# Kernel optimization log

Measured on AMD Instinct MI355X. Metric: run time of the kernel, lower is better.

The kernel has to match this reference:

```python
import jax, jax.numpy as jnp
import numpy as np

B, T, IN_DIM = 128, 4096, 13
UNITS, MOTOR = 64, 6
LAYERS = [35, 23, 6]   # AutoNCP(64, 6): inter / command / motor neurons
_SPLITS = [35, 58]     # cumulative layer boundaries inside the 64-unit state


def setup_inputs() -> dict:
    keys = iter(jax.random.split(jax.random.key(0), 64))
    def rn(shape, s=0.1):
        return jax.random.normal(next(keys), shape, dtype=jnp.float32) * s
    inp = {"x": jax.random.normal(next(keys), (B, T, IN_DIM), dtype=jnp.float32)}
    # mixed-memory LSTM cell (ncps: input_map has bias, recurrent_map does not)
    inp["lstm_wi"] = rn((4 * UNITS, IN_DIM))
    inp["lstm_wh"] = rn((4 * UNITS, UNITS))
    inp["lstm_b"] = rn((4 * UNITS,))
    # wired CfC layers: ff1/ff2/time_a/time_b acting on concat([input, h])
    in_dims = [IN_DIM] + LAYERS[:-1]
    for i, (d, h) in enumerate(zip(in_dims, LAYERS)):
        for nm in ("w1", "w2", "wa", "wb"):
            inp[f"cfc{i}_{nm}"] = rn((h, d + h))
        for nm in ("b1", "b2", "ba", "bb"):
            inp[f"cfc{i}_{nm}"] = rn((h,))
    inp["gyro_w1"] = rn((32, MOTOR)); inp["gyro_b1"] = rn((32,))
    inp["gyro_w2"] = rn((3, 32));     inp["gyro_b2"] = rn((3,))
    inp["acc_w1"] = rn((32, MOTOR));  inp["acc_b1"] = rn((32,))
    inp["acc_w2"] = rn((3, 32));      inp["acc_b2"] = rn((3,))
    inp["unc_w1"] = rn((16, MOTOR));  inp["unc_b1"] = rn((16,))
    inp["unc_w2"] = rn((6, 16));      inp["unc_b2"] = rn((6,))
    return inp


def _cfc_step(inp, h, p):
    """ncps CfCCell, mode='default', no backbone, ts = 1.0."""
    W1, b1, W2, b2, Wa, ba, Wb, bb = p
    z = jnp.concatenate([inp, h], axis=-1)            # (B, in+hid)
    ff1 = jnp.tanh(z @ W1.T + b1)
    ff2 = jnp.tanh(z @ W2.T + b2)
    t = jax.nn.sigmoid((z @ Wa.T + ba) + (z @ Wb.T + bb))  # t_a*ts + t_b, ts==1
    return ff1 * (1.0 - t) + t * ff2


def reference(x, lstm_wi, lstm_wh, lstm_b,
              cfc0_w1, cfc0_b1, cfc0_w2, cfc0_b2, cfc0_wa, cfc0_ba, cfc0_wb, cfc0_bb,
              cfc1_w1, cfc1_b1, cfc1_w2, cfc1_b2, cfc1_wa, cfc1_ba, cfc1_wb, cfc1_bb,
              cfc2_w1, cfc2_b1, cfc2_w2, cfc2_b2, cfc2_wa, cfc2_ba, cfc2_wb, cfc2_bb,
              gyro_w1, gyro_b1, gyro_w2, gyro_b2,
              acc_w1, acc_b1, acc_w2, acc_b2,
              unc_w1, unc_b1, unc_w2, unc_b2):
    layer_params = (
        (cfc0_w1, cfc0_b1, cfc0_w2, cfc0_b2, cfc0_wa, cfc0_ba, cfc0_wb, cfc0_bb),
        (cfc1_w1, cfc1_b1, cfc1_w2, cfc1_b2, cfc1_wa, cfc1_ba, cfc1_wb, cfc1_bb),
        (cfc2_w1, cfc2_b1, cfc2_w2, cfc2_b2, cfc2_wa, cfc2_ba, cfc2_wb, cfc2_bb),
    )

    def step(carry, xt):  # xt: (B, 13)
        h, c = carry
        # mixed-memory LSTM over the full 64-unit state (forget gate +1.0)
        zg = xt @ lstm_wi.T + lstm_b + h @ lstm_wh.T
        ia, ig, fg, og = jnp.split(zg, 4, axis=-1)
        c_new = c * jax.nn.sigmoid(fg + 1.0) + jnp.tanh(ia) * jax.nn.sigmoid(ig)
        h_lstm = jnp.tanh(c_new) * jax.nn.sigmoid(og)
        # wired CfC: inter -> command -> motor, each fed previous layer's output
        hs = jnp.split(h_lstm, _SPLITS, axis=-1)
        inp = xt
        new_hs = []
        for hi, p in zip(hs, layer_params):
            inp = _cfc_step(inp, hi, p)
            new_hs.append(inp)
        return (jnp.concatenate(new_hs, axis=-1), c_new), inp  # motor out (B,6)

    Bsz = x.shape[0]
    h0 = jnp.zeros((Bsz, UNITS), x.dtype)
    c0 = jnp.zeros((Bsz, UNITS), x.dtype)
    _, outs = jax.lax.scan(step, (h0, c0), jnp.swapaxes(x, 0, 1))
    cfc_out = jnp.swapaxes(outs, 0, 1)  # (B, T, 6)

    gyro = jnp.tanh(cfc_out @ gyro_w1.T + gyro_b1) @ gyro_w2.T + gyro_b2
    acc = jnp.tanh(cfc_out @ acc_w1.T + acc_b1) @ acc_w2.T + acc_b2
    pred = jnp.concatenate([gyro, acc], axis=-1)                      # (B, T, 6)
    unc = jax.nn.softplus(
        jax.nn.relu(cfc_out @ unc_w1.T + unc_b1) @ unc_w2.T + unc_b2)  # (B, T, 6)
    return pred, unc
```

## Files before the change

kernel.cpp:

```cpp
#include <hip/hip_runtime.h>
#include <math.h>

#define BATCH 128
#define TSTEPS 4096
#define INDIM 13


__device__ __forceinline__ float fsig(float x) {
    return __builtin_amdgcn_rcpf(1.f + __expf(-x));
}
__device__ __forceinline__ float ftanh(float x) {
    float s = fsig(x + x);
    return s + s - 1.f;
}
__device__ __forceinline__ float fsoftplus(float x) {
    return (x > 15.f) ? x : __logf(1.f + __expf(x));
}

#define BFLY(a) { a += __shfl_xor(a, 1, 64); a += __shfl_xor(a, 2, 64); }

#define FMA4(acc, W, q, zv) { acc += zv.x * W##_##q##_0; acc += zv.y * W##_##q##_1; \
                              acc += zv.z * W##_##q##_2; acc += zv.w * W##_##q##_3; }

__global__ __attribute__((amdgpu_flat_work_group_size(256, 256),
                          amdgpu_waves_per_eu(1, 1)))
void rnn_kernel(const float* __restrict__ x,
                const float* __restrict__ lstm_wi, const float* __restrict__ lstm_wh,
                const float* __restrict__ lstm_b,
                const float* __restrict__ c0w1, const float* __restrict__ c0w2,
                const float* __restrict__ c0wa, const float* __restrict__ c0wb,
                const float* __restrict__ c0b1, const float* __restrict__ c0b2,
                const float* __restrict__ c0ba, const float* __restrict__ c0bb,
                const float* __restrict__ c1w1, const float* __restrict__ c1w2,
                const float* __restrict__ c1wa, const float* __restrict__ c1wb,
                const float* __restrict__ c1b1, const float* __restrict__ c1b2,
                const float* __restrict__ c1ba, const float* __restrict__ c1bb,
                const float* __restrict__ c2w1, const float* __restrict__ c2w2,
                const float* __restrict__ c2wa, const float* __restrict__ c2wb,
                const float* __restrict__ c2b1, const float* __restrict__ c2b2,
                const float* __restrict__ c2ba, const float* __restrict__ c2bb,
                float* __restrict__ out)
{
    const int bb = blockIdx.x;
    const int t  = threadIdx.x;
    const int g  = t & 3;
    const int u  = t >> 2;

    __shared__ __align__(16) float smem[224];
    float* zL = smem;
    float* z0 = smem + 80;
    float* z1 = smem + 128;
    float* z2 = smem + 192;

    const long xbase = (long)bb * TSTEPS * INDIM;
    const long obase = (long)bb * TSTEPS * 6;

    auto lwf = [&](int A, int c) -> float {
        int r = A * 64 + u;
        return (c < 13) ? lstm_wi[r * 13 + c]
             : (c < 77) ? lstm_wh[r * 64 + (c - 13)] : 0.f;
    };
#define DEF_WL(A,q) \
    float wl##A##_##q##_0 = lwf(A, 20*g + 4*q + 0); \
    float wl##A##_##q##_1 = lwf(A, 20*g + 4*q + 1); \
    float wl##A##_##q##_2 = lwf(A, 20*g + 4*q + 2); \
    float wl##A##_##q##_3 = lwf(A, 20*g + 4*q + 3);
    DEF_WL(0,0) DEF_WL(0,1) DEF_WL(0,2) DEF_WL(0,3) DEF_WL(0,4)
    DEF_WL(1,0) DEF_WL(1,1) DEF_WL(1,2) DEF_WL(1,3) DEF_WL(1,4)
    DEF_WL(2,0) DEF_WL(2,1) DEF_WL(2,2) DEF_WL(2,3) DEF_WL(2,4)
    DEF_WL(3,0) DEF_WL(3,1) DEF_WL(3,2) DEF_WL(3,3) DEF_WL(3,4)
#undef DEF_WL
    const float bL0 = lstm_b[u];
    const float bL1 = lstm_b[64 + u];
    const float bL2 = lstm_b[128 + u];
    const float bL3 = lstm_b[192 + u];

    const int grp = (t < 140) ? 0 : (t < 232) ? 1 : 2;
    const int row = (grp == 0) ? u : (grp == 1) ? (u - 35) : (u - 58);
    const int rl  = (grp == 0) ? 48 : (grp == 1) ? 58 : 29;
    const int cb  = (grp == 0) ? 12 * g : (grp == 1) ? 16 * g : 8 * g;
    const float *W0p, *W1p, *W2p, *W3p;
    float bC0, bC1, bC2, bC3;
    if (grp == 0) {
        W0p = c0w1 + row * 48; W1p = c0w2 + row * 48;
        W2p = c0wa + row * 48; W3p = c0wb + row * 48;
        bC0 = c0b1[row]; bC1 = c0b2[row]; bC2 = c0ba[row]; bC3 = c0bb[row];
    } else if (grp == 1) {
        W0p = c1w1 + row * 58; W1p = c1w2 + row * 58;
        W2p = c1wa + row * 58; W3p = c1wb + row * 58;
        bC0 = c1b1[row]; bC1 = c1b2[row]; bC2 = c1ba[row]; bC3 = c1bb[row];
    } else {
        W0p = c2w1 + row * 29; W1p = c2w2 + row * 29;
        W2p = c2wa + row * 29; W3p = c2wb + row * 29;
        bC0 = c2b1[row]; bC1 = c2b2[row]; bC2 = c2ba[row]; bC3 = c2bb[row];
    }
    auto cwf = [&](const float* W, int c) -> float {
        int cc = cb + c;
        return (cc < rl) ? W[cc] : 0.f;
    };
#define DEF_WC(A,q) \
    float wc##A##_##q##_0 = cwf(W##A##p, 4*q + 0); \
    float wc##A##_##q##_1 = cwf(W##A##p, 4*q + 1); \
    float wc##A##_##q##_2 = cwf(W##A##p, 4*q + 2); \
    float wc##A##_##q##_3 = cwf(W##A##p, 4*q + 3);
    DEF_WC(0,0) DEF_WC(0,1) DEF_WC(0,2) DEF_WC(0,3)
    DEF_WC(1,0) DEF_WC(1,1) DEF_WC(1,2) DEF_WC(1,3)
    DEF_WC(2,0) DEF_WC(2,1) DEF_WC(2,2) DEF_WC(2,3)
    DEF_WC(3,0) DEF_WC(3,1) DEF_WC(3,2) DEF_WC(3,3)
#undef DEF_WC

    const bool pfl = (t >= 96 && t < 109);
    float creg = 0.f;

    if (t >= 13 && t < 224) smem[t] = 0.f;
    if (t < 13)             zL[t] = x[xbase + t];
    __syncthreads();

    #pragma unroll 1
    for (int ts = 0; ts < TSTEPS; ++ts) {
        float xn = 0.f;
        if (pfl && (ts + 1) < TSTEPS)
            xn = x[xbase + (long)(ts + 1) * 13 + (t - 96)];
        if (g == 1 && u < 13) z0[u] = zL[u];
        {
            const float4* zc = (const float4*)(zL + 20 * g);
            float4 q0 = zc[0], q1 = zc[1], q2 = zc[2], q3 = zc[3], q4 = zc[4];
            float a0 = 0.f, a1 = 0.f, a2 = 0.f, a3 = 0.f;
            FMA4(a0, wl0, 0, q0) FMA4(a0, wl0, 1, q1) FMA4(a0, wl0, 2, q2)
            FMA4(a0, wl0, 3, q3) FMA4(a0, wl0, 4, q4)
            FMA4(a1, wl1, 0, q0) FMA4(a1, wl1, 1, q1) FMA4(a1, wl1, 2, q2)
            FMA4(a1, wl1, 3, q3) FMA4(a1, wl1, 4, q4)
            FMA4(a2, wl2, 0, q0) FMA4(a2, wl2, 1, q1) FMA4(a2, wl2, 2, q2)
            FMA4(a2, wl2, 3, q3) FMA4(a2, wl2, 4, q4)
            FMA4(a3, wl3, 0, q0) FMA4(a3, wl3, 1, q1) FMA4(a3, wl3, 2, q2)
            FMA4(a3, wl3, 3, q3) FMA4(a3, wl3, 4, q4)
            BFLY(a0) BFLY(a1) BFLY(a2) BFLY(a3)
            a0 += bL0; a1 += bL1; a2 += bL2; a3 += bL3;
            float cn = creg * fsig(a2 + 1.f) + ftanh(a0) * fsig(a1);
            creg = cn;
            float hl = ftanh(cn) * fsig(a3);
            if (g == 0) {
                if (u < 35)      z0[13 + u] = hl;
                else if (u < 58) z1[u]      = hl;
                else             z2[u - 35] = hl;
            }
        }
        __syncthreads();

        if (grp == 0) {
            const float4* zc = (const float4*)(z0 + 12 * g);
            float4 p0 = zc[0], p1 = zc[1], p2 = zc[2];
            float a0 = 0.f, a1 = 0.f, a2 = 0.f, a3 = 0.f;
            FMA4(a0, wc0, 0, p0) FMA4(a0, wc0, 1, p1) FMA4(a0, wc0, 2, p2)
            FMA4(a1, wc1, 0, p0) FMA4(a1, wc1, 1, p1) FMA4(a1, wc1, 2, p2)
            FMA4(a2, wc2, 0, p0) FMA4(a2, wc2, 1, p1) FMA4(a2, wc2, 2, p2)
            FMA4(a3, wc3, 0, p0) FMA4(a3, wc3, 1, p1) FMA4(a3, wc3, 2, p2)
            BFLY(a0) BFLY(a1) BFLY(a2) BFLY(a3)
            a0 += bC0; a1 += bC1; a2 += bC2; a3 += bC3;
            float tg = fsig(a2 + a3);
            float f1 = ftanh(a0), f2 = ftanh(a1);
            float o = f1 + tg * (f2 - f1);
            if (g == 0) { z1[row] = o; zL[13 + row] = o; }
        }
        __syncthreads();

        if (grp == 1) {
            const float4* zc = (const float4*)(z1 + 16 * g);
            float4 p0 = zc[0], p1 = zc[1], p2 = zc[2], p3 = zc[3];
            float a0 = 0.f, a1 = 0.f, a2 = 0.f, a3 = 0.f;
            FMA4(a0, wc0, 0, p0) FMA4(a0, wc0, 1, p1) FMA4(a0, wc0, 2, p2) FMA4(a0, wc0, 3, p3)
            FMA4(a1, wc1, 0, p0) FMA4(a1, wc1, 1, p1) FMA4(a1, wc1, 2, p2) FMA4(a1, wc1, 3, p3)
            FMA4(a2, wc2, 0, p0) FMA4(a2, wc2, 1, p1) FMA4(a2, wc2, 2, p2) FMA4(a2, wc2, 3, p3)
            FMA4(a3, wc3, 0, p0) FMA4(a3, wc3, 1, p1) FMA4(a3, wc3, 2, p2) FMA4(a3, wc3, 3, p3)
            BFLY(a0) BFLY(a1) BFLY(a2) BFLY(a3)
            a0 += bC0; a1 += bC1; a2 += bC2; a3 += bC3;
            float tg = fsig(a2 + a3);
            float f1 = ftanh(a0), f2 = ftanh(a1);
            float o = f1 + tg * (f2 - f1);
            if (g == 0) { z2[row] = o; zL[48 + row] = o; }
        }
        __syncthreads();

        if (grp == 2) {
            const float4* zc = (const float4*)(z2 + 8 * g);
            float4 p0 = zc[0], p1 = zc[1];
            float a0 = 0.f, a1 = 0.f, a2 = 0.f, a3 = 0.f;
            FMA4(a0, wc0, 0, p0) FMA4(a0, wc0, 1, p1)
            FMA4(a1, wc1, 0, p0) FMA4(a1, wc1, 1, p1)
            FMA4(a2, wc2, 0, p0) FMA4(a2, wc2, 1, p1)
            FMA4(a3, wc3, 0, p0) FMA4(a3, wc3, 1, p1)
            BFLY(a0) BFLY(a1) BFLY(a2) BFLY(a3)
            a0 += bC0; a1 += bC1; a2 += bC2; a3 += bC3;
            float tg = fsig(a2 + a3);
            float f1 = ftanh(a0), f2 = ftanh(a1);
            float o = f1 + tg * (f2 - f1);
            if (g == 0) {
                out[obase + (long)ts * 6 + row] = o;
                zL[71 + row] = o;
            }
        } else if (pfl) {
            zL[t - 96] = xn;
        }
        __syncthreads();
    }
}

#define S_GW1 0
#define S_GB1 192
#define S_GW2 224
#define S_GB2 320
#define S_AW1 323
#define S_AB1 515
#define S_AW2 547
#define S_AB2 643
#define S_UW1 646
#define S_UB1 742
#define S_UW2 758
#define S_UB2 854
#define S_TOT 860

__global__ __launch_bounds__(256)
void head_kernel(const float* __restrict__ gw1, const float* __restrict__ gb1,
                 const float* __restrict__ gw2, const float* __restrict__ gb2,
                 const float* __restrict__ aw1, const float* __restrict__ ab1,
                 const float* __restrict__ aw2, const float* __restrict__ ab2,
                 const float* __restrict__ uw1, const float* __restrict__ ub1,
                 const float* __restrict__ uw2, const float* __restrict__ ub2,
                 float* __restrict__ out)
{
    __shared__ float s[S_TOT];
    const int t = threadIdx.x;
    if (t < 192) { s[S_GW1 + t] = gw1[t]; s[S_AW1 + t] = aw1[t]; }
    if (t < 96)  { s[S_GW2 + t] = gw2[t]; s[S_AW2 + t] = aw2[t];
                   s[S_UW1 + t] = uw1[t]; s[S_UW2 + t] = uw2[t]; }
    if (t < 32)  { s[S_GB1 + t] = gb1[t]; s[S_AB1 + t] = ab1[t]; }
    if (t < 16)  { s[S_UB1 + t] = ub1[t]; }
    if (t < 3)   { s[S_GB2 + t] = gb2[t]; s[S_AB2 + t] = ab2[t]; }
    if (t < 6)   { s[S_UB2 + t] = ub2[t]; }
    __syncthreads();

    const long p = (long)blockIdx.x * 256 + t;
    const long base = p * 6;
    float m0 = out[base+0], m1 = out[base+1], m2 = out[base+2];
    float m3 = out[base+3], m4 = out[base+4], m5 = out[base+5];

    float gy0 = s[S_GB2+0], gy1 = s[S_GB2+1], gy2 = s[S_GB2+2];
    float ac0 = s[S_AB2+0], ac1 = s[S_AB2+1], ac2 = s[S_AB2+2];
    #pragma unroll
    for (int i = 0; i < 32; ++i) {
        float hg = s[S_GB1+i] + s[S_GW1+i*6+0]*m0 + s[S_GW1+i*6+1]*m1
                 + s[S_GW1+i*6+2]*m2 + s[S_GW1+i*6+3]*m3
                 + s[S_GW1+i*6+4]*m4 + s[S_GW1+i*6+5]*m5;
        hg = ftanh(hg);
        gy0 += s[S_GW2+i]*hg; gy1 += s[S_GW2+32+i]*hg; gy2 += s[S_GW2+64+i]*hg;
        float ha = s[S_AB1+i] + s[S_AW1+i*6+0]*m0 + s[S_AW1+i*6+1]*m1
                 + s[S_AW1+i*6+2]*m2 + s[S_AW1+i*6+3]*m3
                 + s[S_AW1+i*6+4]*m4 + s[S_AW1+i*6+5]*m5;
        ha = ftanh(ha);
        ac0 += s[S_AW2+i]*ha; ac1 += s[S_AW2+32+i]*ha; ac2 += s[S_AW2+64+i]*ha;
    }
    float u0 = s[S_UB2+0], u1 = s[S_UB2+1], u2 = s[S_UB2+2];
    float u3 = s[S_UB2+3], u4 = s[S_UB2+4], u5 = s[S_UB2+5];
    #pragma unroll
    for (int i = 0; i < 16; ++i) {
        float hu = s[S_UB1+i] + s[S_UW1+i*6+0]*m0 + s[S_UW1+i*6+1]*m1
                 + s[S_UW1+i*6+2]*m2 + s[S_UW1+i*6+3]*m3
                 + s[S_UW1+i*6+4]*m4 + s[S_UW1+i*6+5]*m5;
        hu = fmaxf(hu, 0.f);
        u0 += s[S_UW2+i]*hu;      u1 += s[S_UW2+16+i]*hu; u2 += s[S_UW2+32+i]*hu;
        u3 += s[S_UW2+48+i]*hu;   u4 += s[S_UW2+64+i]*hu; u5 += s[S_UW2+80+i]*hu;
    }
    out[base+0] = gy0; out[base+1] = gy1; out[base+2] = gy2;
    out[base+3] = ac0; out[base+4] = ac1; out[base+5] = ac2;
    const long uoff = (long)BATCH * TSTEPS * 6;
    out[uoff+base+0] = fsoftplus(u0); out[uoff+base+1] = fsoftplus(u1);
    out[uoff+base+2] = fsoftplus(u2); out[uoff+base+3] = fsoftplus(u3);
    out[uoff+base+4] = fsoftplus(u4); out[uoff+base+5] = fsoftplus(u5);
}

extern "C" void kernel_launch(void* const* d_in, const int* in_sizes, int n_in,
                              void* d_out, int out_size, void* d_ws, size_t ws_size,
                              hipStream_t stream) {
    const float* x       = (const float*)d_in[0];
    const float* lstm_wi = (const float*)d_in[1];
    const float* lstm_wh = (const float*)d_in[2];
    const float* lstm_b  = (const float*)d_in[3];
    const float* c0w1 = (const float*)d_in[4];
    const float* c0w2 = (const float*)d_in[5];
    const float* c0wa = (const float*)d_in[6];
    const float* c0wb = (const float*)d_in[7];
    const float* c0b1 = (const float*)d_in[8];
    const float* c0b2 = (const float*)d_in[9];
    const float* c0ba = (const float*)d_in[10];
    const float* c0bb = (const float*)d_in[11];
    const float* c1w1 = (const float*)d_in[12];
    const float* c1w2 = (const float*)d_in[13];
    const float* c1wa = (const float*)d_in[14];
    const float* c1wb = (const float*)d_in[15];
    const float* c1b1 = (const float*)d_in[16];
    const float* c1b2 = (const float*)d_in[17];
    const float* c1ba = (const float*)d_in[18];
    const float* c1bb = (const float*)d_in[19];
    const float* c2w1 = (const float*)d_in[20];
    const float* c2w2 = (const float*)d_in[21];
    const float* c2wa = (const float*)d_in[22];
    const float* c2wb = (const float*)d_in[23];
    const float* c2b1 = (const float*)d_in[24];
    const float* c2b2 = (const float*)d_in[25];
    const float* c2ba = (const float*)d_in[26];
    const float* c2bb = (const float*)d_in[27];
    const float* gw1 = (const float*)d_in[28];
    const float* gb1 = (const float*)d_in[29];
    const float* gw2 = (const float*)d_in[30];
    const float* gb2 = (const float*)d_in[31];
    const float* aw1 = (const float*)d_in[32];
    const float* ab1 = (const float*)d_in[33];
    const float* aw2 = (const float*)d_in[34];
    const float* ab2 = (const float*)d_in[35];
    const float* uw1 = (const float*)d_in[36];
    const float* ub1 = (const float*)d_in[37];
    const float* uw2 = (const float*)d_in[38];
    const float* ub2 = (const float*)d_in[39];
    float* out = (float*)d_out;

    rnn_kernel<<<BATCH, 256, 0, stream>>>(x, lstm_wi, lstm_wh, lstm_b,
        c0w1, c0w2, c0wa, c0wb, c0b1, c0b2, c0ba, c0bb,
        c1w1, c1w2, c1wa, c1wb, c1b1, c1b2, c1ba, c1bb,
        c2w1, c2w2, c2wa, c2wb, c2b1, c2b2, c2ba, c2bb, out);

    head_kernel<<<(BATCH * TSTEPS) / 256, 256, 0, stream>>>(
        gw1, gb1, gw2, gb2, aw1, ab1, aw2, ab2, uw1, ub1, uw2, ub2, out);
}
```

Before: 6.448 ms.

## Split each unit's dot products across 8 lanes with DPP/swizzle reductions

Doubles the block to 512 threads so each hidden unit's LSTM and CfC dot products are split across 8 lanes instead of 4. This shortens the serial FMA chain per lane in every recurrent step. The 3-step shuffle reduction uses DPP quad permutes plus a ds_swizzle in place of __shfl_xor. The cost is twice as many waves synchronising at each of the four barriers per timestep, and one extra reduction stage.

```diff
diff --git a/kernel.cpp b/kernel.cpp
--- a/kernel.cpp
+++ b/kernel.cpp
@@ -17,13 +17,24 @@
     return (x > 15.f) ? x : __logf(1.f + __expf(x));
 }
 
-#define BFLY(a) { a += __shfl_xor(a, 1, 64); a += __shfl_xor(a, 2, 64); }
+__device__ __forceinline__ float qxor1(float v) {
+    return __int_as_float(__builtin_amdgcn_update_dpp(
+        0, __float_as_int(v), 0xB1, 0xF, 0xF, true));
+}
+__device__ __forceinline__ float qxor2(float v) {
+    return __int_as_float(__builtin_amdgcn_update_dpp(
+        0, __float_as_int(v), 0x4E, 0xF, 0xF, true));
+}
+__device__ __forceinline__ float sxor4(float v) {
+    return __int_as_float(__builtin_amdgcn_ds_swizzle(
+        __float_as_int(v), 0x101F));
+}
+#define BFLY8(a) { a += sxor4(a); a += qxor2(a); a += qxor1(a); }
 
 #define FMA4(acc, W, q, zv) { acc += zv.x * W##_##q##_0; acc += zv.y * W##_##q##_1; \
                               acc += zv.z * W##_##q##_2; acc += zv.w * W##_##q##_3; }
 
-__global__ __attribute__((amdgpu_flat_work_group_size(256, 256),
-                          amdgpu_waves_per_eu(1, 1)))
+__global__ __launch_bounds__(512, 2)
 void rnn_kernel(const float* __restrict__ x,
                 const float* __restrict__ lstm_wi, const float* __restrict__ lstm_wh,
                 const float* __restrict__ lstm_b,
@@ -43,14 +54,14 @@
 {
     const int bb = blockIdx.x;
     const int t  = threadIdx.x;
-    const int g  = t & 3;
-    const int u  = t >> 2;
-
-    __shared__ __align__(16) float smem[224];
+    const int k  = t & 7;
+    const int u  = t >> 3;
+
+    __shared__ __align__(16) float smem[256];
     float* zL = smem;
-    float* z0 = smem + 80;
-    float* z1 = smem + 128;
-    float* z2 = smem + 192;
+    float* z0 = smem + 96;
+    float* z1 = smem + 160;
+    float* z2 = smem + 224;
 
     const long xbase = (long)bb * TSTEPS * INDIM;
     const long obase = (long)bb * TSTEPS * 6;
@@ -61,24 +72,25 @@
              : (c < 77) ? lstm_wh[r * 64 + (c - 13)] : 0.f;
     };
 #define DEF_WL(A,q) \
-    float wl##A##_##q##_0 = lwf(A, 20*g + 4*q + 0); \
-    float wl##A##_##q##_1 = lwf(A, 20*g + 4*q + 1); \
-    float wl##A##_##q##_2 = lwf(A, 20*g + 4*q + 2); \
-    float wl##A##_##q##_3 = lwf(A, 20*g + 4*q + 3);
-    DEF_WL(0,0) DEF_WL(0,1) DEF_WL(0,2) DEF_WL(0,3) DEF_WL(0,4)
-    DEF_WL(1,0) DEF_WL(1,1) DEF_WL(1,2) DEF_WL(1,3) DEF_WL(1,4)
-    DEF_WL(2,0) DEF_WL(2,1) DEF_WL(2,2) DEF_WL(2,3) DEF_WL(2,4)
-    DEF_WL(3,0) DEF_WL(3,1) DEF_WL(3,2) DEF_WL(3,3) DEF_WL(3,4)
+    float wl##A##_##q##_0 = lwf(A, 12*k + 4*q + 0); \
+    float wl##A##_##q##_1 = lwf(A, 12*k + 4*q + 1); \
+    float wl##A##_##q##_2 = lwf(A, 12*k + 4*q + 2); \
+    float wl##A##_##q##_3 = lwf(A, 12*k + 4*q + 3);
+    DEF_WL(0,0) DEF_WL(0,1) DEF_WL(0,2)
+    DEF_WL(1,0) DEF_WL(1,1) DEF_WL(1,2)
+    DEF_WL(2,0) DEF_WL(2,1) DEF_WL(2,2)
+    DEF_WL(3,0) DEF_WL(3,1) DEF_WL(3,2)
 #undef DEF_WL
     const float bL0 = lstm_b[u];
     const float bL1 = lstm_b[64 + u];
     const float bL2 = lstm_b[128 + u];
     const float bL3 = lstm_b[192 + u];
 
-    const int grp = (t < 140) ? 0 : (t < 232) ? 1 : 2;
-    const int row = (grp == 0) ? u : (grp == 1) ? (u - 35) : (u - 58);
-    const int rl  = (grp == 0) ? 48 : (grp == 1) ? 58 : 29;
-    const int cb  = (grp == 0) ? 12 * g : (grp == 1) ? 16 * g : 8 * g;
+    const int grp  = (u < 35) ? 0 : (u < 58) ? 1 : 2;
+    const int row  = (grp == 0) ? u : (grp == 1) ? (u - 35) : (u - 58);
+    const int rl   = (grp == 0) ? 48 : (grp == 1) ? 58 : 29;
+    const int clen = (grp == 2) ? 4 : 8;
+    const int cb   = (grp == 2) ? 4 * k : 8 * k;
     const float *W0p, *W1p, *W2p, *W3p;
     float bC0, bC1, bC2, bC3;
     if (grp == 0) {
@@ -96,50 +108,47 @@
     }
     auto cwf = [&](const float* W, int c) -> float {
         int cc = cb + c;
-        return (cc < rl) ? W[cc] : 0.f;
+        return (c < clen && cc < rl) ? W[cc] : 0.f;
     };
 #define DEF_WC(A,q) \
     float wc##A##_##q##_0 = cwf(W##A##p, 4*q + 0); \
     float wc##A##_##q##_1 = cwf(W##A##p, 4*q + 1); \
     float wc##A##_##q##_2 = cwf(W##A##p, 4*q + 2); \
     float wc##A##_##q##_3 = cwf(W##A##p, 4*q + 3);
-    DEF_WC(0,0) DEF_WC(0,1) DEF_WC(0,2) DEF_WC(0,3)
-    DEF_WC(1,0) DEF_WC(1,1) DEF_WC(1,2) DEF_WC(1,3)
-    DEF_WC(2,0) DEF_WC(2,1) DEF_WC(2,2) DEF_WC(2,3)
-    DEF_WC(3,0) DEF_WC(3,1) DEF_WC(3,2) DEF_WC(3,3)
+    DEF_WC(0,0) DEF_WC(0,1)
+    DEF_WC(1,0) DEF_WC(1,1)
+    DEF_WC(2,0) DEF_WC(2,1)
+    DEF_WC(3,0) DEF_WC(3,1)
 #undef DEF_WC
 
-    const bool pfl = (t >= 96 && t < 109);
+    const bool pfl = (t >= 128 && t < 141);
     float creg = 0.f;
 
-    if (t >= 13 && t < 224) smem[t] = 0.f;
-    if (t < 13)             zL[t] = x[xbase + t];
+    if (t < 256) smem[t] = 0.f;
+    __syncthreads();
+    if (t < 13) zL[t] = x[xbase + t];
     __syncthreads();
 
     #pragma unroll 1
     for (int ts = 0; ts < TSTEPS; ++ts) {
         float xn = 0.f;
         if (pfl && (ts + 1) < TSTEPS)
-            xn = x[xbase + (long)(ts + 1) * 13 + (t - 96)];
-        if (g == 1 && u < 13) z0[u] = zL[u];
+            xn = x[xbase + (long)(ts + 1) * 13 + (t - 128)];
+        if (t >= 256 && t < 269) z0[t - 256] = zL[t - 256];
         {
-            const float4* zc = (const float4*)(zL + 20 * g);
-            float4 q0 = zc[0], q1 = zc[1], q2 = zc[2], q3 = zc[3], q4 = zc[4];
+            const float4* zc = (const float4*)(zL + 12 * k);
+            float4 q0 = zc[0], q1 = zc[1], q2 = zc[2];
             float a0 = 0.f, a1 = 0.f, a2 = 0.f, a3 = 0.f;
             FMA4(a0, wl0, 0, q0) FMA4(a0, wl0, 1, q1) FMA4(a0, wl0, 2, q2)
-            FMA4(a0, wl0, 3, q3) FMA4(a0, wl0, 4, q4)
             FMA4(a1, wl1, 0, q0) FMA4(a1, wl1, 1, q1) FMA4(a1, wl1, 2, q2)
-            FMA4(a1, wl1, 3, q3) FMA4(a1, wl1, 4, q4)
             FMA4(a2, wl2, 0, q0) FMA4(a2, wl2, 1, q1) FMA4(a2, wl2, 2, q2)
-            FMA4(a2, wl2, 3, q3) FMA4(a2, wl2, 4, q4)
             FMA4(a3, wl3, 0, q0) FMA4(a3, wl3, 1, q1) FMA4(a3, wl3, 2, q2)
-            FMA4(a3, wl3, 3, q3) FMA4(a3, wl3, 4, q4)
-            BFLY(a0) BFLY(a1) BFLY(a2) BFLY(a3)
+            BFLY8(a0) BFLY8(a1) BFLY8(a2) BFLY8(a3)
             a0 += bL0; a1 += bL1; a2 += bL2; a3 += bL3;
             float cn = creg * fsig(a2 + 1.f) + ftanh(a0) * fsig(a1);
             creg = cn;
             float hl = ftanh(cn) * fsig(a3);
-            if (g == 0) {
+            if (k == 0) {
                 if (u < 35)      z0[13 + u] = hl;
                 else if (u < 58) z1[u]      = hl;
                 else             z2[u - 35] = hl;
@@ -148,58 +157,58 @@
         __syncthreads();
 
         if (grp == 0) {
-            const float4* zc = (const float4*)(z0 + 12 * g);
-            float4 p0 = zc[0], p1 = zc[1], p2 = zc[2];
-            float a0 = 0.f, a1 = 0.f, a2 = 0.f, a3 = 0.f;
-            FMA4(a0, wc0, 0, p0) FMA4(a0, wc0, 1, p1) FMA4(a0, wc0, 2, p2)
-            FMA4(a1, wc1, 0, p0) FMA4(a1, wc1, 1, p1) FMA4(a1, wc1, 2, p2)
-            FMA4(a2, wc2, 0, p0) FMA4(a2, wc2, 1, p1) FMA4(a2, wc2, 2, p2)
-            FMA4(a3, wc3, 0, p0) FMA4(a3, wc3, 1, p1) FMA4(a3, wc3, 2, p2)
-            BFLY(a0) BFLY(a1) BFLY(a2) BFLY(a3)
-            a0 += bC0; a1 += bC1; a2 += bC2; a3 += bC3;
-            float tg = fsig(a2 + a3);
-            float f1 = ftanh(a0), f2 = ftanh(a1);
-            float o = f1 + tg * (f2 - f1);
-            if (g == 0) { z1[row] = o; zL[13 + row] = o; }
-        }
-        __syncthreads();
-
-        if (grp == 1) {
-            const float4* zc = (const float4*)(z1 + 16 * g);
-            float4 p0 = zc[0], p1 = zc[1], p2 = zc[2], p3 = zc[3];
-            float a0 = 0.f, a1 = 0.f, a2 = 0.f, a3 = 0.f;
-            FMA4(a0, wc0, 0, p0) FMA4(a0, wc0, 1, p1) FMA4(a0, wc0, 2, p2) FMA4(a0, wc0, 3, p3)
-            FMA4(a1, wc1, 0, p0) FMA4(a1, wc1, 1, p1) FMA4(a1, wc1, 2, p2) FMA4(a1, wc1, 3, p3)
-            FMA4(a2, wc2, 0, p0) FMA4(a2, wc2, 1, p1) FMA4(a2, wc2, 2, p2) FMA4(a2, wc2, 3, p3)
-            FMA4(a3, wc3, 0, p0) FMA4(a3, wc3, 1, p1) FMA4(a3, wc3, 2, p2) FMA4(a3, wc3, 3, p3)
-            BFLY(a0) BFLY(a1) BFLY(a2) BFLY(a3)
-            a0 += bC0; a1 += bC1; a2 += bC2; a3 += bC3;
-            float tg = fsig(a2 + a3);
-            float f1 = ftanh(a0), f2 = ftanh(a1);
-            float o = f1 + tg * (f2 - f1);
-            if (g == 0) { z2[row] = o; zL[48 + row] = o; }
-        }
-        __syncthreads();
-
-        if (grp == 2) {
-            const float4* zc = (const float4*)(z2 + 8 * g);
+            const float4* zc = (const float4*)(z0 + 8 * k);
             float4 p0 = zc[0], p1 = zc[1];
             float a0 = 0.f, a1 = 0.f, a2 = 0.f, a3 = 0.f;
             FMA4(a0, wc0, 0, p0) FMA4(a0, wc0, 1, p1)
             FMA4(a1, wc1, 0, p0) FMA4(a1, wc1, 1, p1)
             FMA4(a2, wc2, 0, p0) FMA4(a2, wc2, 1, p1)
             FMA4(a3, wc3, 0, p0) FMA4(a3, wc3, 1, p1)
-            BFLY(a0) BFLY(a1) BFLY(a2) BFLY(a3)
+            BFLY8(a0) BFLY8(a1) BFLY8(a2) BFLY8(a3)
             a0 += bC0; a1 += bC1; a2 += bC2; a3 += bC3;
             float tg = fsig(a2 + a3);
             float f1 = ftanh(a0), f2 = ftanh(a1);
             float o = f1 + tg * (f2 - f1);
-            if (g == 0) {
+            if (k == 0) { z1[row] = o; zL[13 + row] = o; }
+        }
+        __syncthreads();
+
+        if (grp == 1) {
+            const float4* zc = (const float4*)(z1 + 8 * k);
+            float4 p0 = zc[0], p1 = zc[1];
+            float a0 = 0.f, a1 = 0.f, a2 = 0.f, a3 = 0.f;
+            FMA4(a0, wc0, 0, p0) FMA4(a0, wc0, 1, p1)
+            FMA4(a1, wc1, 0, p0) FMA4(a1, wc1, 1, p1)
+            FMA4(a2, wc2, 0, p0) FMA4(a2, wc2, 1, p1)
+            FMA4(a3, wc3, 0, p0) FMA4(a3, wc3, 1, p1)
+            BFLY8(a0) BFLY8(a1) BFLY8(a2) BFLY8(a3)
+            a0 += bC0; a1 += bC1; a2 += bC2; a3 += bC3;
+            float tg = fsig(a2 + a3);
+            float f1 = ftanh(a0), f2 = ftanh(a1);
+            float o = f1 + tg * (f2 - f1);
+            if (k == 0) { z2[row] = o; zL[48 + row] = o; }
+        }
+        __syncthreads();
+
+        if (grp == 2) {
+            const float4* zc = (const float4*)(z2 + 4 * k);
+            float4 p0 = zc[0];
+            float a0 = 0.f, a1 = 0.f, a2 = 0.f, a3 = 0.f;
+            FMA4(a0, wc0, 0, p0)
+            FMA4(a1, wc1, 0, p0)
+            FMA4(a2, wc2, 0, p0)
+            FMA4(a3, wc3, 0, p0)
+            BFLY8(a0) BFLY8(a1) BFLY8(a2) BFLY8(a3)
+            a0 += bC0; a1 += bC1; a2 += bC2; a3 += bC3;
+            float tg = fsig(a2 + a3);
+            float f1 = ftanh(a0), f2 = ftanh(a1);
+            float o = f1 + tg * (f2 - f1);
+            if (k == 0) {
                 out[obase + (long)ts * 6 + row] = o;
                 zL[71 + row] = o;
             }
         } else if (pfl) {
-            zL[t - 96] = xn;
+            zL[t - 128] = xn;
         }
         __syncthreads();
     }
@@ -323,7 +332,7 @@
     const float* ub2 = (const float*)d_in[39];
     float* out = (float*)d_out;
 
-    rnn_kernel<<<BATCH, 256, 0, stream>>>(x, lstm_wi, lstm_wh, lstm_b,
+    rnn_kernel<<<BATCH, 512, 0, stream>>>(x, lstm_wi, lstm_wh, lstm_b,
         c0w1, c0w2, c0wa, c0wb, c0b1, c0b2, c0ba, c0bb,
         c1w1, c1w2, c1wa, c1wb, c1b1, c1b2, c1ba, c1bb,
         c2w1, c2w2, c2wa, c2wb, c2b1, c2b2, c2ba, c2bb, out);
```

New measurement: 5.845 ms. 1.1x faster.
